# Kernel tuning notes

Hardware: AMD Instinct MI355X
Metric: run time of the kernel (lower is better)

The kernel has to match this reference:

```python
import jax, jax.numpy as jnp
import numpy as np

K = 65536          # memory bank size
P = 4096           # partition_size
D = 256            # out_dim
E = 2              # num_experts_per_concept
SMOOTH = 0.1
NUM_TASKS = 1
B = 4096


def setup_inputs() -> dict:
    key = jax.random.key(0)
    k1, k2, k3 = jax.random.split(key, 3)
    queue = jax.random.normal(k1, (D, K), dtype=jnp.float32)
    queue = queue / jnp.linalg.norm(queue, axis=0, keepdims=True)  # normalize(dim=0)
    return {
        "student_embeds": jax.random.normal(k2, (B, D), dtype=jnp.float32),
        "teacher_embeds": jax.random.normal(k3, (B, D), dtype=jnp.float32),
        "queue": queue,
        "student_temp": 0.1,
        "teacher_temp": 0.04,
    }


def _one_task(queue, student_embeds, teacher_embeds, student_temp, teacher_temp, key):
    kperm, ksel = jax.random.split(key)
    # random partition of the bank (torch.randperm + split)
    perm = jax.random.permutation(kperm, K)
    part_idx, mem_idx = perm[:P], perm[P:]
    part = queue[:, part_idx]                      # [D, P]
    mem = queue[:, mem_idx]                        # [D, K-P]
    Kmp = K - P

    sims = part.T @ mem                            # [P, K-P]
    neigh_scores, neigh_idx = jax.lax.top_k(sims, E - 1)  # [P, E-1]

    # append self index (offset into concatenated [mem | part]) and 1-smoothing score
    idx_ = jnp.concatenate([neigh_idx, (Kmp + jnp.arange(P))[:, None]], axis=1)          # [P, E]
    scores_ = jnp.concatenate(
        [neigh_scores, jnp.full((P, 1), 1.0 - SMOOTH, dtype=sims.dtype)], axis=1)        # [P, E]

    # low_energy selection: multinomial(weights, P//2, replacement=False)
    P2 = P // 2
    m = jnp.mean(neigh_scores, axis=-1)            # [P]
    sample_means = jnp.abs(m)
    sample_stds = m                                 # (faithful to source: same quantity)
    coef = (sample_stds / (sample_means + 1e-8)) * (1.0 + 1.0 / (4.0 * Kmp))
    weights = 1.0 / coef                            # [P]
    # Gumbel top-k == multinomial without replacement proportional to weights
    gumbel = jax.random.gumbel(ksel, (P,))
    sel = jax.lax.top_k(jnp.log(weights) + gumbel, P2)[1]   # [P2]
    idx_ = idx_[sel]                                # [P2, E]
    scores_ = scores_[sel]                          # [P2, E]

    embeds_ = jnp.concatenate([mem, part], axis=1)  # [D, K]
    pne = embeds_[:, idx_.reshape(-1)]              # [D, P2*E] partition_neigh_embeddings

    sf = scores_.reshape(-1)                        # [P2*E]
    smooth_val = (1.0 - sf) / (P2 - 1)              # [P2*E]
    # partition_labels = arange(P).repeat_interleave(E)[:P2*E] == repeat(arange(P2), E)
    labels = jnp.repeat(jnp.arange(P2), E)          # [P2*E]
    M = jnp.broadcast_to(smooth_val[:, None], (P2 * E, P2))
    M = M.at[jnp.arange(P2 * E), labels].set(sf)    # scatter_ on dim 1
    M = M / M.sum(-1, keepdims=True)                # row-normalize

    s_probs = jax.nn.softmax(student_embeds @ pne / student_temp, axis=-1) @ M  # [B, P2]
    t_probs = jax.nn.softmax(teacher_embeds @ pne / teacher_temp, axis=-1) @ M  # [B, P2]
    return s_probs, t_probs


def reference(student_embeds, teacher_embeds, queue, student_temp, teacher_temp):
    base = jax.random.key(42)  # internal RNG (torch.randperm / multinomial equivalents)
    s_list, t_list = [], []
    for i in range(NUM_TASKS):
        s, t = _one_task(queue, student_embeds, teacher_embeds,
                         student_temp, teacher_temp, jax.random.fold_in(base, i))
        s_list.append(s)
        t_list.append(t)
    return jnp.stack(s_list), jnp.stack(t_list)  # each [NUM_TASKS, B, P//2]
```

## Files before the change

kernel.cpp:

```cpp
#include <hip/hip_runtime.h>
#include <cstdint>
#include <cmath>
#include <cstring>
#include <vector>
#include <algorithm>
#include <utility>

#define KTOT 65536
#define PP   4096
#define DD   256
#define KMP  61440
#define P2   2048
#define BB   4096
#define NPB  512
#define INVALID_C 0xFFFFFFFFu

static inline void tf2x32(uint32_t k0, uint32_t k1, uint32_t x0, uint32_t x1,
                          uint32_t* o0, uint32_t* o1) {
  static const uint32_t rot[2][4] = {{13u,15u,26u,6u},{17u,29u,16u,24u}};
  uint32_t ks[3] = {k0, k1, 0x1BD11BDAu ^ k0 ^ k1};
  uint32_t v0 = x0 + ks[0], v1 = x1 + ks[1];
  for (int i = 0; i < 5; ++i) {
    const uint32_t* r = rot[i & 1];
    for (int j = 0; j < 4; ++j) {
      v0 += v1;
      v1 = (v1 << r[j]) | (v1 >> (32u - r[j]));
      v1 ^= v0;
    }
    v0 += ks[(i + 1) % 3];
    v1 += ks[(i + 2) % 3] + (uint32_t)(i + 1);
  }
  *o0 = v0; *o1 = v1;
}

static inline uint32_t tf_bits32(uint32_t k0, uint32_t k1, uint32_t i) {
  uint32_t a, b;
  tf2x32(k0, k1, 0u, i, &a, &b);
  return a ^ b;
}

static uint32_t h_mem_idx[KMP];
static uint32_t h_pos_in_mem[KTOT];
static uint32_t h_partsel[P2];

static void host_prepare() {
  uint32_t f0, f1; tf2x32(0u, 42u, 0u, 0u, &f0, &f1);
  uint32_t kperm0, kperm1, ksel0, ksel1;
  tf2x32(f0, f1, 0u, 0u, &kperm0, &kperm1);
  tf2x32(f0, f1, 0u, 1u, &ksel0, &ksel1);

  std::vector<uint32_t> perm(KTOT);
  for (uint32_t i = 0; i < KTOT; ++i) perm[i] = i;
  std::vector<std::pair<uint32_t,uint32_t>> kv(KTOT);
  uint32_t key0 = kperm0, key1 = kperm1;
  for (int round = 0; round < 2; ++round) {
    uint32_t nk0, nk1, sk0, sk1;
    tf2x32(key0, key1, 0u, 0u, &nk0, &nk1);
    tf2x32(key0, key1, 0u, 1u, &sk0, &sk1);
    key0 = nk0; key1 = nk1;
    for (uint32_t i = 0; i < KTOT; ++i) {
      kv[i].first  = tf_bits32(sk0, sk1, i);
      kv[i].second = perm[i];
    }
    std::stable_sort(kv.begin(), kv.end(),
        [](const std::pair<uint32_t,uint32_t>& a,
           const std::pair<uint32_t,uint32_t>& b){ return a.first < b.first; });
    for (uint32_t i = 0; i < KTOT; ++i) perm[i] = kv[i].second;
  }
  static uint32_t part_idx[PP];
  for (int i = 0; i < PP;  ++i) part_idx[i] = perm[i];
  for (int i = 0; i < KMP; ++i) h_mem_idx[i] = perm[PP + i];
  for (int i = 0; i < KTOT; ++i) h_pos_in_mem[i] = INVALID_C;
  for (uint32_t c = 0; c < KMP; ++c) h_pos_in_mem[h_mem_idx[c]] = c;

  static float sval[PP];
  float c1f = (float)(1.0 + 1.0/(4.0*(double)KMP));
  float L0  = logf(1.0f / c1f);
  for (uint32_t i = 0; i < PP; ++i) {
    uint32_t bits = tf_bits32(ksel0, ksel1, i);
    uint32_t fb = (bits >> 9) | 0x3F800000u;
    float f; memcpy(&f, &fb, 4);
    f -= 1.0f;
    float u = (f == 0.0f) ? 1.17549435e-38f : f;
    float g = -logf(-logf(u));
    sval[i] = L0 + g;
  }
  static uint32_t order[PP];
  for (uint32_t i = 0; i < PP; ++i) order[i] = i;
  std::sort(order, order + PP, [](uint32_t a, uint32_t b){
    if (sval[a] != sval[b]) return sval[a] > sval[b];
    return a < b;
  });
  for (int k = 0; k < P2; ++k) h_partsel[k] = part_idx[order[k]];
}

static const bool _host_tables_ready = (host_prepare(), true);

typedef __attribute__((ext_vector_type(8))) short bf16x8;
typedef __attribute__((ext_vector_type(4))) float f32x4;

__device__ inline unsigned short f2bf(float x) {
  union { float f; uint32_t u; } v; v.f = x;
  return (unsigned short)((v.u + 0x7FFFu + ((v.u >> 16) & 1u)) >> 16);
}

__device__ inline void gload16(const unsigned short* g, unsigned short* l) {
  __builtin_amdgcn_global_load_lds(
      (const __attribute__((address_space(1))) unsigned int*)g,
      (__attribute__((address_space(3))) unsigned int*)l, 16, 0, 0);
}

__device__ __host__ inline int swz_g(int row) {
  return ((row >> 1) & 3) | (((row >> 3) & 1) << 3);
}
__device__ __host__ inline int swz(int row, int d) {
  return d ^ (swz_g(row) << 1);
}

__global__ __launch_bounds__(256)
void transpose_bf16(const float* __restrict__ queue, unsigned short* __restrict__ BhT) {
  __shared__ float t[64][65];
  const int tid = threadIdx.x;
  const int c4 = (tid & 15) * 4, r = tid >> 4;
  const int n0 = blockIdx.x * 64, d0 = blockIdx.y * 64;
#pragma unroll
  for (int i = 0; i < 4; ++i) {
    int d = r + i * 16;
    float4 v = *(const float4*)&queue[(d0 + d) * KTOT + n0 + c4];
    t[d][c4 + 0] = v.x; t[d][c4 + 1] = v.y; t[d][c4 + 2] = v.z; t[d][c4 + 3] = v.w;
  }
  __syncthreads();
#pragma unroll
  for (int i = 0; i < 4; ++i) {
    int n = r + i * 16;
    uint32_t lo = (uint32_t)f2bf(t[c4 + 0][n]) | ((uint32_t)f2bf(t[c4 + 1][n]) << 16);
    uint32_t hi = (uint32_t)f2bf(t[c4 + 2][n]) | ((uint32_t)f2bf(t[c4 + 3][n]) << 16);
    const int row = n0 + n;
    const int g = swz_g(row);
    const int pos = ((d0 + c4) ^ (g << 1)) & ~3;
    uint2 w;
    w.x = (g & 1) ? hi : lo;
    w.y = (g & 1) ? lo : hi;
    *(uint2*)&BhT[row * DD + pos] = w;
  }
}

__global__ __launch_bounds__(256)
void gather_A(const float* __restrict__ queue, const uint32_t* __restrict__ psel,
              float* __restrict__ Apart, unsigned short* __restrict__ AhT) {
  int p = blockIdx.x, d = threadIdx.x;
  float q = queue[d * KTOT + (int)psel[p]];
  Apart[p * DD + d] = q;
  AhT[p * DD + swz(p, d)] = f2bf(q);
}

__global__ __launch_bounds__(256)
void mfma_argmax(const unsigned short* __restrict__ AhT,
                 const unsigned short* __restrict__ BhT,
                 const uint32_t* __restrict__ pos_in_mem,
                 float* __restrict__ pv2, uint32_t* __restrict__ pc2) {
  __shared__ union SM {
    struct { unsigned short As[2][128][32]; unsigned short Bs[2][128][32]; } s;
    struct { float rv[128][33]; uint32_t ri[128][33]; } r;
  } sm;
  const int tid = threadIdx.x;

  const int flat = blockIdx.y * NPB + blockIdx.x;
  const int xcd = flat & 7, job = flat >> 3;
  const int nt = (xcd << 6) + (job >> 4);
  const int mt = job & 15;
  const int m0 = mt * 128, n0 = nt * 128;

  const int wave = tid >> 6, lane = tid & 63;
  const int wm = (wave >> 1) * 64, wn = (wave & 1) * 64;
  const int l15 = lane & 15, quad = lane >> 4;

  uint32_t carr[4];
#pragma unroll
  for (int j = 0; j < 4; ++j) carr[j] = pos_in_mem[n0 + wn + j * 16 + l15];

  const int gsw = swz_g(l15);
  const int o0 = (((quad << 2) | 0) ^ gsw) << 2;
  const int o1 = (((quad << 2) | 1) ^ gsw) << 2;
  const int o2 = (((quad << 2) | 2) ^ gsw) << 2;
  const int o3 = (((quad << 2) | 3) ^ gsw) << 2;

  f32x4 acc[4][4];
#pragma unroll
  for (int i = 0; i < 4; ++i)
#pragma unroll
    for (int j = 0; j < 4; ++j) acc[i][j] = (f32x4){0.f, 0.f, 0.f, 0.f};

  const int r4 = lane >> 2;
  const int c8 = (lane & 3) * 8;
  const unsigned short* gA0 = &AhT[(m0 + wave * 16 + r4) * DD + c8];
  const unsigned short* gA1 = gA0 + 64 * DD;
  const unsigned short* gB0 = &BhT[(n0 + wave * 16 + r4) * DD + c8];
  const unsigned short* gB1 = gB0 + 64 * DD;

  {
    unsigned short* lA = &sm.s.As[0][wave * 16][0];
    unsigned short* lB = &sm.s.Bs[0][wave * 16][0];
    gload16(gA0, lA); gload16(gA1, lA + 64 * 32);
    gload16(gB0, lB); gload16(gB1, lB + 64 * 32);
  }
  __syncthreads();

  for (int t = 0; t < 8; ++t) {
    const int cur = t & 1;
    if (t < 7) {
      const int k0 = (t + 1) * 32;
      unsigned short* lA = &sm.s.As[cur ^ 1][wave * 16][0];
      unsigned short* lB = &sm.s.Bs[cur ^ 1][wave * 16][0];
      gload16(gA0 + k0, lA); gload16(gA1 + k0, lA + 64 * 32);
      gload16(gB0 + k0, lB); gload16(gB1 + k0, lB + 64 * 32);
    }
    bf16x8 a[4], b[4];
#pragma unroll
    for (int i = 0; i < 4; ++i) {
      const char* rb = (const char*)&sm.s.As[cur][wm + i * 16 + l15][0];
      union { uint32_t u[4]; bf16x8 v; } f;
      f.u[0] = *(const uint32_t*)(rb + o0);
      f.u[1] = *(const uint32_t*)(rb + o1);
      f.u[2] = *(const uint32_t*)(rb + o2);
      f.u[3] = *(const uint32_t*)(rb + o3);
      a[i] = f.v;
    }
#pragma unroll
    for (int j = 0; j < 4; ++j) {
      const char* rb = (const char*)&sm.s.Bs[cur][wn + j * 16 + l15][0];
      union { uint32_t u[4]; bf16x8 v; } f;
      f.u[0] = *(const uint32_t*)(rb + o0);
      f.u[1] = *(const uint32_t*)(rb + o1);
      f.u[2] = *(const uint32_t*)(rb + o2);
      f.u[3] = *(const uint32_t*)(rb + o3);
      b[j] = f.v;
    }
#pragma unroll
    for (int i = 0; i < 4; ++i)
#pragma unroll
      for (int j = 0; j < 4; ++j)
        acc[i][j] = __builtin_amdgcn_mfma_f32_16x16x32_bf16(a[i], b[j], acc[i][j], 0, 0, 0);
    __syncthreads();
  }

#pragma unroll
  for (int i = 0; i < 4; ++i)
#pragma unroll
    for (int r = 0; r < 4; ++r) {
      float bv = -INFINITY; uint32_t bc = INVALID_C;
#pragma unroll
      for (int j = 0; j < 4; ++j) {
        float v = acc[i][j][r]; uint32_t c = carr[j];
        if (c != INVALID_C && (v > bv || (v == bv && c < bc))) { bv = v; bc = c; }
      }
      int row = wm + i * 16 + quad * 4 + r;
      sm.r.rv[row][(wave & 1) * 16 + l15] = bv;
      sm.r.ri[row][(wave & 1) * 16 + l15] = bc;
    }
  __syncthreads();
  if (tid < 128) {
    float v1 = -INFINITY, v2 = -INFINITY; uint32_t c1 = INVALID_C, c2 = INVALID_C;
#pragma unroll 4
    for (int s = 0; s < 32; ++s) {
      float v = sm.r.rv[tid][s]; uint32_t c = sm.r.ri[tid][s];
      if (c == INVALID_C) continue;
      if (v > v1 || (v == v1 && c < c1)) { v2 = v1; c2 = c1; v1 = v; c1 = c; }
      else if (v > v2 || (v == v2 && c < c2)) { v2 = v; c2 = c; }
    }
    int base = (m0 + tid) * (NPB * 2) + nt * 2;
    pv2[base] = v1;     pc2[base] = c1;
    pv2[base + 1] = v2; pc2[base + 1] = c2;
  }
}

#define EPS_W 0.01f
__global__ __launch_bounds__(256)
void argmax_rescore(const float* __restrict__ pv2, const uint32_t* __restrict__ pc2,
                    const float* __restrict__ Apart, const float* __restrict__ queue,
                    const uint32_t* __restrict__ mem_idx,
                    float* __restrict__ nval, uint32_t* __restrict__ nc) {
  __shared__ float red[256];
  __shared__ uint32_t cand[32];
  __shared__ int cnt;
  const int row = blockIdx.x, tid = threadIdx.x;

  float m = -INFINITY;
  for (int e = tid; e < NPB * 2; e += 256) m = fmaxf(m, pv2[row * (NPB * 2) + e]);
  red[tid] = m; __syncthreads();
  for (int s = 128; s > 0; s >>= 1) {
    if (tid < s) red[tid] = fmaxf(red[tid], red[tid + s]);
    __syncthreads();
  }
  const float M = red[0];
  if (tid == 0) cnt = 0;
  __syncthreads();
  for (int e = tid; e < NPB * 2; e += 256) {
    float v = pv2[row * (NPB * 2) + e]; uint32_t c = pc2[row * (NPB * 2) + e];
    if (c != INVALID_C && v >= M - EPS_W) {
      int k = atomicAdd(&cnt, 1);
      if (k < 32) cand[k] = c;
    }
  }
  __syncthreads();
  const int ncand = min(cnt, 32);
  __shared__ float bestv_s; __shared__ uint32_t bestc_s;
  if (tid == 0) { bestv_s = -INFINITY; bestc_s = INVALID_C; }
  __syncthreads();
  const float av = Apart[row * DD + tid];
  for (int k = 0; k < ncand; ++k) {
    uint32_t c = cand[k];
    int n = (int)mem_idx[c];
    red[tid] = av * queue[tid * KTOT + n];
    __syncthreads();
    for (int s = 128; s > 0; s >>= 1) {
      if (tid < s) red[tid] += red[tid + s];
      __syncthreads();
    }
    if (tid == 0) {
      float sc = red[0];
      if (sc > bestv_s || (sc == bestv_s && c < bestc_s)) { bestv_s = sc; bestc_s = c; }
    }
    __syncthreads();
  }
  if (tid == 0) { nval[row] = bestv_s; nc[row] = bestc_s; }
}

__global__ __launch_bounds__(256)
void prep(const uint32_t* __restrict__ nc, const float* __restrict__ nval,
          const uint32_t* __restrict__ mem_idx, const uint32_t* __restrict__ partsel,
          uint32_t* __restrict__ g_idx, float* __restrict__ svp, float* __restrict__ dp) {
  int k = blockIdx.x * 256 + threadIdx.x;
  if (k >= P2) return;
  uint32_t c = nc[k];
  float sf0 = nval[k];
  float sf1 = 0.9f;
  g_idx[2 * k]     = mem_idx[c];
  g_idx[2 * k + 1] = partsel[k];
  float sv0 = (1.0f - sf0) / 2047.0f;
  float sv1 = (1.0f - sf1) / 2047.0f;
  float rs0 = sf0 + 2047.0f * sv0;
  float rs1 = sf1 + 2047.0f * sv1;
  svp[2 * k]     = sv0 / rs0;  dp[2 * k]     = (sf0 - sv0) / rs0;
  svp[2 * k + 1] = sv1 / rs1;  dp[2 * k + 1] = (sf1 - sv1) / rs1;
}

__global__ __launch_bounds__(256)
void cvt_A(const float* __restrict__ S, const float* __restrict__ T,
           unsigned short* __restrict__ AhS, unsigned short* __restrict__ AlS,
           unsigned short* __restrict__ AhT, unsigned short* __restrict__ AlT) {
  int b = blockIdx.x, d = threadIdx.x;
  const float* src = (b < BB) ? S : T;
  unsigned short* oh = (b < BB) ? AhS : AhT;
  unsigned short* ol = (b < BB) ? AlS : AlT;
  int row = b & (BB - 1);
  float v = src[row * DD + d];
  unsigned short hb = f2bf(v);
  float hf = __uint_as_float((uint32_t)hb << 16);
  unsigned short lb = f2bf(v - hf);
  int o = row * DD + swz(row, d);
  oh[o] = hb;
  ol[o] = lb;
}

__global__ __launch_bounds__(256)
void gather_B(const float* __restrict__ queue, const uint32_t* __restrict__ g_idx,
              unsigned short* __restrict__ Bh, unsigned short* __restrict__ Bl) {
  int r = blockIdx.x, d = threadIdx.x;
  float v = queue[d * KTOT + (int)g_idx[r]];
  unsigned short hb = f2bf(v);
  float hf = __uint_as_float((uint32_t)hb << 16);
  unsigned short lb = f2bf(v - hf);
  int o = r * DD + swz(r, d);
  Bh[o] = hb;
  Bl[o] = lb;
}

__global__ __launch_bounds__(256)
void gemm_split(const unsigned short* __restrict__ Ah,
                const unsigned short* __restrict__ Al,
                const unsigned short* __restrict__ Bh,
                const unsigned short* __restrict__ Bl,
                float* __restrict__ Fo) {
  __shared__ struct { unsigned short As[2][128][32]; unsigned short Bs[2][128][32]; } sm;
  const int tid = threadIdx.x;
  const int m0 = blockIdx.y * 128, n0 = blockIdx.x * 128;
  const int wave = tid >> 6, lane = tid & 63;
  const int wm = (wave >> 1) * 64, wn = (wave & 1) * 64;
  const int l15 = lane & 15, quad = lane >> 4;

  const int gsw = swz_g(l15);
  const int o0 = (((quad << 2) | 0) ^ gsw) << 2;
  const int o1 = (((quad << 2) | 1) ^ gsw) << 2;
  const int o2 = (((quad << 2) | 2) ^ gsw) << 2;
  const int o3 = (((quad << 2) | 3) ^ gsw) << 2;

  f32x4 acc[4][4];
#pragma unroll
  for (int i = 0; i < 4; ++i)
#pragma unroll
    for (int j = 0; j < 4; ++j) acc[i][j] = (f32x4){0.f, 0.f, 0.f, 0.f};

  const int r4 = lane >> 2;
  const int c8 = (lane & 3) * 8;
  const int aoff = (m0 + wave * 16 + r4) * DD + c8;
  const int boff = (n0 + wave * 16 + r4) * DD + c8;

  {
    unsigned short* lA = &sm.As[0][wave * 16][0];
    unsigned short* lB = &sm.Bs[0][wave * 16][0];
    gload16(Ah + aoff, lA); gload16(Ah + aoff + 64 * DD, lA + 64 * 32);
    gload16(Bh + boff, lB); gload16(Bh + boff + 64 * DD, lB + 64 * 32);
  }
  __syncthreads();

#pragma unroll 2
  for (int t = 0; t < 24; ++t) {
    const int cur = t & 1;
    if (t < 23) {
      const int tn = t + 1;
      const int p = tn >> 3, k0 = (tn & 7) * 32;
      const unsigned short* ga = ((p == 2) ? Al : Ah) + aoff + k0;
      const unsigned short* gb = ((p == 1) ? Bl : Bh) + boff + k0;
      unsigned short* lA = &sm.As[cur ^ 1][wave * 16][0];
      unsigned short* lB = &sm.Bs[cur ^ 1][wave * 16][0];
      gload16(ga, lA); gload16(ga + 64 * DD, lA + 64 * 32);
      gload16(gb, lB); gload16(gb + 64 * DD, lB + 64 * 32);
    }
    bf16x8 a[4], b[4];
#pragma unroll
    for (int i = 0; i < 4; ++i) {
      const char* rb = (const char*)&sm.As[cur][wm + i * 16 + l15][0];
      union { uint32_t u[4]; bf16x8 v; } f;
      f.u[0] = *(const uint32_t*)(rb + o0);
      f.u[1] = *(const uint32_t*)(rb + o1);
      f.u[2] = *(const uint32_t*)(rb + o2);
      f.u[3] = *(const uint32_t*)(rb + o3);
      a[i] = f.v;
    }
#pragma unroll
    for (int j = 0; j < 4; ++j) {
      const char* rb = (const char*)&sm.Bs[cur][wn + j * 16 + l15][0];
      union { uint32_t u[4]; bf16x8 v; } f;
      f.u[0] = *(const uint32_t*)(rb + o0);
      f.u[1] = *(const uint32_t*)(rb + o1);
      f.u[2] = *(const uint32_t*)(rb + o2);
      f.u[3] = *(const uint32_t*)(rb + o3);
      b[j] = f.v;
    }
#pragma unroll
    for (int i = 0; i < 4; ++i)
#pragma unroll
      for (int j = 0; j < 4; ++j)
        acc[i][j] = __builtin_amdgcn_mfma_f32_16x16x32_bf16(a[i], b[j], acc[i][j], 0, 0, 0);
    __syncthreads();
  }

#pragma unroll
  for (int i = 0; i < 4; ++i)
#pragma unroll
    for (int j = 0; j < 4; ++j)
#pragma unroll
      for (int r = 0; r < 4; ++r)
        Fo[(m0 + wm + i * 16 + quad * 4 + r) * PP + n0 + wn + j * 16 + l15] = acc[i][j][r];
}

__global__ __launch_bounds__(256)
void softmax_out(const float* __restrict__ F, const float* __restrict__ temp_ptr,
                 const float* __restrict__ svp, const float* __restrict__ dp,
                 float* __restrict__ out) {
  __shared__ float e[PP];
  __shared__ float red[256];
  int b = blockIdx.x, tid = threadIdx.x;
  const float invtemp = 1.0f / temp_ptr[0];
  float lmax = -INFINITY;
  for (int r = tid; r < PP; r += 256) {
    float l = F[b * PP + r] * invtemp;
    e[r] = l;
    lmax = fmaxf(lmax, l);
  }
  red[tid] = lmax; __syncthreads();
  for (int s = 128; s > 0; s >>= 1) {
    if (tid < s) red[tid] = fmaxf(red[tid], red[tid + s]);
    __syncthreads();
  }
  lmax = red[0]; __syncthreads();

  float z = 0.0f, sacc = 0.0f;
  for (int r = tid; r < PP; r += 256) {
    float ev = __expf(e[r] - lmax);
    e[r] = ev;
    z += ev;
    sacc = fmaf(ev, svp[r], sacc);
  }
  red[tid] = z; __syncthreads();
  for (int s = 128; s > 0; s >>= 1) {
    if (tid < s) red[tid] += red[tid + s];
    __syncthreads();
  }
  z = red[0]; __syncthreads();
  red[tid] = sacc; __syncthreads();
  for (int s = 128; s > 0; s >>= 1) {
    if (tid < s) red[tid] += red[tid + s];
    __syncthreads();
  }
  sacc = red[0]; __syncthreads();

  float invz = 1.0f / z;
  for (int j = tid; j < P2; j += 256) {
    float v = sacc + e[2 * j] * dp[2 * j] + e[2 * j + 1] * dp[2 * j + 1];
    out[b * P2 + j] = v * invz;
  }
}

#define OFF_BHT      0u
#define OFF_PV2      33554432u
#define OFF_PC2      41943040u
#define OFF_AHT      50331648u
#define OFF_APART    51380224u
#define OFF_F        0u
#define OFF_BH       33554432u
#define OFF_BL       35651584u
#define OFF_AHS      37748736u
#define OFF_ALS      39845888u
#define OFF_AHT2     41943040u
#define OFF_ALT2     44040192u
#define OFF_SVP      71303168u
#define OFF_DP       71319552u
#define OFF_GIDX     71335936u
#define OFF_NVAL     71352320u
#define OFF_NC       71360512u
#define OFF_UP_MEM   71368704u
#define OFF_UP_POS   71614464u
#define OFF_UP_PSEL  71876608u

extern "C" void kernel_launch(void* const* d_in, const int* in_sizes, int n_in,
                              void* d_out, int out_size, void* d_ws, size_t ws_size,
                              hipStream_t stream) {
  (void)in_sizes; (void)n_in; (void)out_size; (void)ws_size;
  (void)_host_tables_ready;
  const float* d_student = (const float*)d_in[0];
  const float* d_teacher = (const float*)d_in[1];
  const float* d_queue   = (const float*)d_in[2];
  const float* d_stemp   = (const float*)d_in[3];
  const float* d_ttemp   = (const float*)d_in[4];
  float* out = (float*)d_out;
  char* ws = (char*)d_ws;

  unsigned short* BhT   = (unsigned short*)(ws + OFF_BHT);
  float*          pv2   = (float*)(ws + OFF_PV2);
  uint32_t*       pc2   = (uint32_t*)(ws + OFF_PC2);
  unsigned short* AhT   = (unsigned short*)(ws + OFF_AHT);
  float*          Apart = (float*)(ws + OFF_APART);
  float*          F     = (float*)(ws + OFF_F);
  unsigned short* Bh    = (unsigned short*)(ws + OFF_BH);
  unsigned short* Bl    = (unsigned short*)(ws + OFF_BL);
  unsigned short* AhS   = (unsigned short*)(ws + OFF_AHS);
  unsigned short* AlS   = (unsigned short*)(ws + OFF_ALS);
  unsigned short* AhT2  = (unsigned short*)(ws + OFF_AHT2);
  unsigned short* AlT2  = (unsigned short*)(ws + OFF_ALT2);
  float*          svp   = (float*)(ws + OFF_SVP);
  float*          dp    = (float*)(ws + OFF_DP);
  uint32_t*       g_idx = (uint32_t*)(ws + OFF_GIDX);
  float*          nval  = (float*)(ws + OFF_NVAL);
  uint32_t*       nc    = (uint32_t*)(ws + OFF_NC);
  uint32_t*       dMemIdx = (uint32_t*)(ws + OFF_UP_MEM);
  uint32_t*       dPosMem = (uint32_t*)(ws + OFF_UP_POS);
  uint32_t*       dPSel   = (uint32_t*)(ws + OFF_UP_PSEL);

  hipMemcpyAsync(dMemIdx, h_mem_idx,    KMP  * sizeof(uint32_t), hipMemcpyHostToDevice, stream);
  hipMemcpyAsync(dPosMem, h_pos_in_mem, KTOT * sizeof(uint32_t), hipMemcpyHostToDevice, stream);
  hipMemcpyAsync(dPSel,   h_partsel,    P2   * sizeof(uint32_t), hipMemcpyHostToDevice, stream);

  transpose_bf16<<<dim3(KTOT / 64, DD / 64), 256, 0, stream>>>(d_queue, BhT);
  gather_A<<<P2, 256, 0, stream>>>(d_queue, dPSel, Apart, AhT);
  mfma_argmax<<<dim3(NPB, P2 / 128), 256, 0, stream>>>(AhT, BhT, dPosMem, pv2, pc2);
  argmax_rescore<<<P2, 256, 0, stream>>>(pv2, pc2, Apart, d_queue, dMemIdx, nval, nc);
  prep<<<P2 / 256, 256, 0, stream>>>(nc, nval, dMemIdx, dPSel, g_idx, svp, dp);

  cvt_A<<<2 * BB, 256, 0, stream>>>(d_student, d_teacher, AhS, AlS, AhT2, AlT2);
  gather_B<<<PP, 256, 0, stream>>>(d_queue, g_idx, Bh, Bl);

  for (int half = 0; half < 2; ++half) {
    gemm_split<<<dim3(PP / 128, 2048 / 128), 256, 0, stream>>>(
        AhS + (size_t)half * 2048 * DD, AlS + (size_t)half * 2048 * DD, Bh, Bl, F);
    softmax_out<<<2048, 256, 0, stream>>>(F, d_stemp, svp, dp,
        out + (size_t)half * 2048 * P2);
  }
  for (int half = 0; half < 2; ++half) {
    gemm_split<<<dim3(PP / 128, 2048 / 128), 256, 0, stream>>>(
        AhT2 + (size_t)half * 2048 * DD, AlT2 + (size_t)half * 2048 * DD, Bh, Bl, F);
    softmax_out<<<2048, 256, 0, stream>>>(F, d_ttemp, svp, dp,
        out + (size_t)BB * P2 + (size_t)half * 2048 * P2);
  }
}
```

Baseline: 531.5 us.

## Merge host uploads into one pinned copy and use wave-shuffle reductions

Packs the three host index tables into one contiguous pinned buffer and uploads them with a single async copy instead of three pageable copies. It also replaces the shared-memory tree reductions in argmax_rescore and softmax_out with wave shuffles plus a four-entry cross-wave combine, which removes many barriers. softmax_out now keeps its logits in registers, and the MFMA k-loop is fully unrolled. The single copy relies on the device regions dMemIdx, dPosMem and dPSel being laid out contiguously in the same order as the host buffer.

```diff
diff --git a/kernel.cpp b/kernel.cpp
--- a/kernel.cpp
+++ b/kernel.cpp
@@ -39,9 +39,10 @@
   return a ^ b;
 }
 
-static uint32_t h_mem_idx[KMP];
-static uint32_t h_pos_in_mem[KTOT];
-static uint32_t h_partsel[P2];
+static uint32_t h_upload[KMP + KTOT + P2];
+static uint32_t* const h_mem_idx    = h_upload;
+static uint32_t* const h_pos_in_mem = h_upload + KMP;
+static uint32_t* const h_partsel    = h_upload + KMP + KTOT;
 
 static void host_prepare() {
   uint32_t f0, f1; tf2x32(0u, 42u, 0u, 0u, &f0, &f1);
@@ -92,6 +93,8 @@
     return a < b;
   });
   for (int k = 0; k < P2; ++k) h_partsel[k] = part_idx[order[k]];
+
+  (void)hipHostRegister((void*)h_upload, sizeof(h_upload), hipHostRegisterDefault);
 }
 
 static const bool _host_tables_ready = (host_prepare(), true);
@@ -108,6 +111,17 @@
   __builtin_amdgcn_global_load_lds(
       (const __attribute__((address_space(1))) unsigned int*)g,
       (__attribute__((address_space(3))) unsigned int*)l, 16, 0, 0);
+}
+
+__device__ inline float wave_max(float v) {
+#pragma unroll
+  for (int off = 32; off > 0; off >>= 1) v = fmaxf(v, __shfl_xor(v, off, 64));
+  return v;
+}
+__device__ inline float wave_sum(float v) {
+#pragma unroll
+  for (int off = 32; off > 0; off >>= 1) v += __shfl_xor(v, off, 64);
+  return v;
 }
 
 __device__ __host__ inline int swz_g(int row) {
@@ -206,6 +220,7 @@
   }
   __syncthreads();
 
+#pragma unroll
   for (int t = 0; t < 8; ++t) {
     const int cur = t & 1;
     if (t < 7) {
@@ -280,21 +295,20 @@
                     const float* __restrict__ Apart, const float* __restrict__ queue,
                     const uint32_t* __restrict__ mem_idx,
                     float* __restrict__ nval, uint32_t* __restrict__ nc) {
-  __shared__ float red[256];
+  __shared__ float wr[4];
   __shared__ uint32_t cand[32];
   __shared__ int cnt;
+  __shared__ float bestv_s; __shared__ uint32_t bestc_s;
   const int row = blockIdx.x, tid = threadIdx.x;
-
+  const int wave = tid >> 6;
+
+  if (tid == 0) { cnt = 0; bestv_s = -INFINITY; bestc_s = INVALID_C; }
   float m = -INFINITY;
   for (int e = tid; e < NPB * 2; e += 256) m = fmaxf(m, pv2[row * (NPB * 2) + e]);
-  red[tid] = m; __syncthreads();
-  for (int s = 128; s > 0; s >>= 1) {
-    if (tid < s) red[tid] = fmaxf(red[tid], red[tid + s]);
-    __syncthreads();
-  }
-  const float M = red[0];
-  if (tid == 0) cnt = 0;
-  __syncthreads();
+  m = wave_max(m);
+  if ((tid & 63) == 0) wr[wave] = m;
+  __syncthreads();
+  const float M = fmaxf(fmaxf(wr[0], wr[1]), fmaxf(wr[2], wr[3]));
   for (int e = tid; e < NPB * 2; e += 256) {
     float v = pv2[row * (NPB * 2) + e]; uint32_t c = pc2[row * (NPB * 2) + e];
     if (c != INVALID_C && v >= M - EPS_W) {
@@ -304,21 +318,15 @@
   }
   __syncthreads();
   const int ncand = min(cnt, 32);
-  __shared__ float bestv_s; __shared__ uint32_t bestc_s;
-  if (tid == 0) { bestv_s = -INFINITY; bestc_s = INVALID_C; }
-  __syncthreads();
   const float av = Apart[row * DD + tid];
   for (int k = 0; k < ncand; ++k) {
     uint32_t c = cand[k];
     int n = (int)mem_idx[c];
-    red[tid] = av * queue[tid * KTOT + n];
+    float p = wave_sum(av * queue[tid * KTOT + n]);
+    if ((tid & 63) == 0) wr[wave] = p;
     __syncthreads();
-    for (int s = 128; s > 0; s >>= 1) {
-      if (tid < s) red[tid] += red[tid + s];
-      __syncthreads();
-    }
     if (tid == 0) {
-      float sc = red[0];
+      float sc = wr[0] + wr[1] + wr[2] + wr[3];
       if (sc > bestv_s || (sc == bestv_s && c < bestc_s)) { bestv_s = sc; bestc_s = c; }
     }
     __syncthreads();
@@ -470,41 +478,38 @@
                  const float* __restrict__ svp, const float* __restrict__ dp,
                  float* __restrict__ out) {
   __shared__ float e[PP];
-  __shared__ float red[256];
+  __shared__ float wrm[4], wrz[4], wrs[4];
   int b = blockIdx.x, tid = threadIdx.x;
+  const int wave = tid >> 6;
   const float invtemp = 1.0f / temp_ptr[0];
+  float lv[PP / 256];
   float lmax = -INFINITY;
-  for (int r = tid; r < PP; r += 256) {
-    float l = F[b * PP + r] * invtemp;
-    e[r] = l;
+#pragma unroll
+  for (int k = 0; k < PP / 256; ++k) {
+    float l = F[b * PP + tid + k * 256] * invtemp;
+    lv[k] = l;
     lmax = fmaxf(lmax, l);
   }
-  red[tid] = lmax; __syncthreads();
-  for (int s = 128; s > 0; s >>= 1) {
-    if (tid < s) red[tid] = fmaxf(red[tid], red[tid + s]);
-    __syncthreads();
-  }
-  lmax = red[0]; __syncthreads();
+  lmax = wave_max(lmax);
+  if ((tid & 63) == 0) wrm[wave] = lmax;
+  __syncthreads();
+  lmax = fmaxf(fmaxf(wrm[0], wrm[1]), fmaxf(wrm[2], wrm[3]));
 
   float z = 0.0f, sacc = 0.0f;
-  for (int r = tid; r < PP; r += 256) {
-    float ev = __expf(e[r] - lmax);
+#pragma unroll
+  for (int k = 0; k < PP / 256; ++k) {
+    int r = tid + k * 256;
+    float ev = __expf(lv[k] - lmax);
     e[r] = ev;
     z += ev;
     sacc = fmaf(ev, svp[r], sacc);
   }
-  red[tid] = z; __syncthreads();
-  for (int s = 128; s > 0; s >>= 1) {
-    if (tid < s) red[tid] += red[tid + s];
-    __syncthreads();
-  }
-  z = red[0]; __syncthreads();
-  red[tid] = sacc; __syncthreads();
-  for (int s = 128; s > 0; s >>= 1) {
-    if (tid < s) red[tid] += red[tid + s];
-    __syncthreads();
-  }
-  sacc = red[0]; __syncthreads();
+  z = wave_sum(z);
+  sacc = wave_sum(sacc);
+  if ((tid & 63) == 0) { wrz[wave] = z; wrs[wave] = sacc; }
+  __syncthreads();
+  z = wrz[0] + wrz[1] + wrz[2] + wrz[3];
+  sacc = wrs[0] + wrs[1] + wrs[2] + wrs[3];
 
   float invz = 1.0f / z;
   for (int j = tid; j < P2; j += 256) {
@@ -568,9 +573,7 @@
   uint32_t*       dPosMem = (uint32_t*)(ws + OFF_UP_POS);
   uint32_t*       dPSel   = (uint32_t*)(ws + OFF_UP_PSEL);
 
-  hipMemcpyAsync(dMemIdx, h_mem_idx,    KMP  * sizeof(uint32_t), hipMemcpyHostToDevice, stream);
-  hipMemcpyAsync(dPosMem, h_pos_in_mem, KTOT * sizeof(uint32_t), hipMemcpyHostToDevice, stream);
-  hipMemcpyAsync(dPSel,   h_partsel,    P2   * sizeof(uint32_t), hipMemcpyHostToDevice, stream);
+  hipMemcpyAsync(dMemIdx, h_upload, sizeof(h_upload), hipMemcpyHostToDevice, stream);
 
   transpose_bf16<<<dim3(KTOT / 64, DD / 64), 256, 0, stream>>>(d_queue, BhT);
   gather_A<<<P2, 256, 0, stream>>>(d_queue, dPSel, Apart, AhT);
```

Measured after the change: 477.4 us. -10.2%, faster.
